# Optimization experiments

Hardware: AMD Instinct MI355X
Metric: run time of the kernel (lower is better)

## Reference

```python
import jax, jax.numpy as jnp
import numpy as np

N_HEADS = 8
N_LEVELS = 1
N_POINTS = 4
D_MODEL = 256
BATCH = 2
H0, W0 = 100, 150
LS = H0 * W0
LQ = 15000


def layer_norm(x, g, b, eps=1e-5):
    m = jnp.mean(x, -1, keepdims=True)
    v = jnp.var(x, -1, keepdims=True)
    return (x - m) * jax.lax.rsqrt(v + eps) * g + b


def bilinear_sample(v, Hl, Wl, loc):
    # v: [N, Hl*Wl, Hh, D] level features; loc in [0,1]: [N, Lq, Hh, P, 2] (x, y)
    Nb, _, Hh, D = v.shape
    Lq, P = loc.shape[1], loc.shape[3]
    x = loc[..., 0] * Wl - 0.5           # align_corners=False grid_sample convention
    y = loc[..., 1] * Hl - 0.5
    x0 = jnp.floor(x); y0 = jnp.floor(y)
    lx = (x - x0).transpose(0, 2, 1, 3)[..., None]   # [N,Hh,Lq,P,1]
    ly = (y - y0).transpose(0, 2, 1, 3)[..., None]
    x0i = x0.astype(jnp.int32); y0i = y0.astype(jnp.int32)
    vh = v.transpose(0, 2, 1, 3)                      # [N,Hh,Hl*Wl,D]

    def gather(xi, yi):
        valid = (xi >= 0) & (xi < Wl) & (yi >= 0) & (yi < Hl)   # zero padding
        idx = jnp.clip(yi, 0, Hl - 1) * Wl + jnp.clip(xi, 0, Wl - 1)
        idxf = idx.transpose(0, 2, 1, 3).reshape(Nb, Hh, Lq * P)
        g = jnp.take_along_axis(vh, idxf[..., None], axis=2).reshape(Nb, Hh, Lq, P, D)
        return g * valid.transpose(0, 2, 1, 3)[..., None]

    g00 = gather(x0i, y0i)
    g10 = gather(x0i + 1, y0i)
    g01 = gather(x0i, y0i + 1)
    g11 = gather(x0i + 1, y0i + 1)
    return (g00 * (1 - lx) * (1 - ly) + g10 * lx * (1 - ly)
            + g01 * (1 - lx) * ly + g11 * lx * ly)   # [N,Hh,Lq,P,D]


def ms_deform_attn(q, reference_points, src, shapes_np, starts_np, padding_mask,
                   W_val, b_val, W_off, b_off, W_attn, b_attn, W_out, b_out):
    Nb, Lq, C = q.shape
    Hh, D, L, P = N_HEADS, C // N_HEADS, N_LEVELS, N_POINTS
    value = src @ W_val + b_val
    value = jnp.where(padding_mask[..., None], 0.0, value).reshape(Nb, -1, Hh, D)
    offsets = (q @ W_off + b_off).reshape(Nb, Lq, Hh, L, P, 2)
    aw = jax.nn.softmax((q @ W_attn + b_attn).reshape(Nb, Lq, Hh, L * P), -1)
    aw = aw.reshape(Nb, Lq, Hh, L, P)
    # offset normalizer is (W, H) per level
    norm = jnp.asarray(shapes_np[:, ::-1].copy(), dtype=q.dtype)   # [L,2]
    loc = reference_points[:, :, None, :, None, :] + offsets / norm[None, None, None, :, None, :]
    out = 0.0
    for l in range(L):
        Hl, Wl = int(shapes_np[l, 0]), int(shapes_np[l, 1])
        s = int(starts_np[l])
        sampled = bilinear_sample(value[:, s:s + Hl * Wl], Hl, Wl, loc[:, :, :, l])
        out = out + jnp.sum(sampled * aw[:, :, :, l].transpose(0, 2, 1, 3)[..., None], axis=3)
    out = out.transpose(0, 2, 1, 3).reshape(Nb, Lq, C)
    return out @ W_out + b_out


def reference(tgt, query_pos, src_pos, tgt_spatial_shapes, reference_points,
              depth_reference_points, src, src_spatial_shapes, frame_start_index,
              src_padding_mask,
              W_dsa, b_dsa, g_nds, b_nds, W_off, b_off, W_attn, b_attn,
              W_val, b_val, W_out, b_out, W_csa, b_csa, g_n1, b_n1,
              W_ff, b_ff, g_n3, b_n3):
    ss = np.asarray(src_spatial_shapes)      # static level shapes
    starts = np.asarray(frame_start_index)
    # depth scale adaptation
    src_a = layer_norm(src @ W_dsa + b_dsa, g_nds, b_nds)
    q = tgt + query_pos
    tgt2 = ms_deform_attn(q, reference_points, src_a, ss, starts, src_padding_mask,
                          W_val, b_val, W_off, b_off, W_attn, b_attn, W_out, b_out)
    tgt2 = tgt2 @ W_csa + b_csa
    t = layer_norm(tgt + tgt2, g_n1, b_n1)
    # FFN: single linear d_model->d_model with exact GELU (per source code)
    ff = jax.nn.gelu(t @ W_ff + b_ff, approximate=False)
    return layer_norm(t + ff, g_n3, b_n3)


def setup_inputs() -> dict:
    key = jax.random.key(0)
    ks = jax.random.split(key, 24)
    C = D_MODEL
    Hh, L, P = N_HEADS, N_LEVELS, N_POINTS

    def lin(k, fin, fout, scale=None):
        s = (1.0 / np.sqrt(fin)) if scale is None else scale
        return (jax.random.normal(k, (fin, fout), jnp.float32) * s).astype(jnp.float32)

    inp = {}
    inp['tgt'] = jax.random.normal(ks[0], (BATCH, LQ, C), jnp.float32)
    inp['query_pos'] = 0.1 * jax.random.normal(ks[1], (BATCH, LQ, C), jnp.float32)
    inp['src_pos'] = 0.1 * jax.random.normal(ks[2], (BATCH, LS, C), jnp.float32)
    inp['tgt_spatial_shapes'] = jnp.array([[H0, W0]], jnp.int32)
    inp['reference_points'] = jax.random.uniform(ks[3], (BATCH, LQ, L, 2), jnp.float32)
    inp['depth_reference_points'] = jax.random.uniform(ks[4], (BATCH, LQ, 1, 2), jnp.float32)
    inp['src'] = jax.random.normal(ks[5], (BATCH, LS, C), jnp.float32)
    inp['src_spatial_shapes'] = jnp.array([[H0, W0]], jnp.int32)
    inp['frame_start_index'] = jnp.array([0], jnp.int32)
    inp['src_padding_mask'] = jnp.zeros((BATCH, LS), jnp.bool_)
    # parameters
    inp['W_dsa'] = lin(ks[6], C, C); inp['b_dsa'] = jnp.zeros((C,), jnp.float32)
    inp['g_nds'] = jnp.ones((C,), jnp.float32); inp['b_nds'] = jnp.zeros((C,), jnp.float32)
    inp['W_off'] = lin(ks[7], C, Hh * L * P * 2, scale=0.01)
    inp['b_off'] = 0.5 * jax.random.normal(ks[8], (Hh * L * P * 2,), jnp.float32)
    inp['W_attn'] = lin(ks[9], C, Hh * L * P)
    inp['b_attn'] = jnp.zeros((Hh * L * P,), jnp.float32)
    inp['W_val'] = lin(ks[10], C, C); inp['b_val'] = jnp.zeros((C,), jnp.float32)
    inp['W_out'] = lin(ks[11], C, C); inp['b_out'] = jnp.zeros((C,), jnp.float32)
    inp['W_csa'] = lin(ks[12], C, C); inp['b_csa'] = jnp.zeros((C,), jnp.float32)
    inp['g_n1'] = jnp.ones((C,), jnp.float32); inp['b_n1'] = jnp.zeros((C,), jnp.float32)
    inp['W_ff'] = lin(ks[13], C, C); inp['b_ff'] = jnp.zeros((C,), jnp.float32)
    inp['g_n3'] = jnp.ones((C,), jnp.float32); inp['b_n3'] = jnp.zeros((C,), jnp.float32)
    return inp
```

## Files before the change

kernel.cpp:

```cpp
#include <hip/hip_runtime.h>
#include <hip/hip_bf16.h>
#include <math.h>

#define LQ   15000
#define LS_  15000
#define NB   2
#define ROWS (NB*LQ)
#define HGT  100
#define WID  150

typedef __attribute__((ext_vector_type(8))) short bf16x8;
typedef __attribute__((ext_vector_type(4))) float f32x4;

__device__ inline short f2bf(float x) {
    __hip_bfloat16 h = __float2bfloat16(x);
    return *reinterpret_cast<short*>(&h);
}
__device__ inline unsigned pack2bf(float a, float b) {
    return ((unsigned)(unsigned short)f2bf(a)) | (((unsigned)(unsigned short)f2bf(b)) << 16);
}
__device__ inline float bf2f(short s) {
    return __uint_as_float(((unsigned)(unsigned short)s) << 16);
}
__device__ inline float gelu_exact(float x) {
    return 0.5f * x * (1.f + erff(x * 0.70710678118654752440f));
}

template<int MODE>
__global__ __launch_bounds__(256) void fused2(
    const void* __restrict__ Ap,
    const short* __restrict__ W1T, const float* __restrict__ bias1,
    const float* __restrict__ res1,
    const float* __restrict__ g1v, const float* __restrict__ b1v,
    const short* __restrict__ W2T, const float* __restrict__ bias2,
    void* __restrict__ Out,
    const unsigned char* __restrict__ mask,
    const float* __restrict__ g2v, const float* __restrict__ b2v,
    int M)
{
    __shared__ short As[64][40];
    __shared__ short Bs[256][40];
    __shared__ short T[64][264];
    __shared__ float s_b1[256], s_g1[256], s_bb1[256], s_b2[256], s_g2[256], s_bb2[256];

    const int tid = threadIdx.x;
    const int bm0 = blockIdx.x * 64;
    const int wave = tid >> 6, lane = tid & 63;
    const int quad = lane >> 4, c = lane & 15;

    s_b1[tid] = bias1[tid];
    s_g1[tid] = g1v[tid]; s_bb1[tid] = b1v[tid];
    s_b2[tid] = bias2[tid];
    if (MODE == 1) { s_g2[tid] = g2v[tid]; s_bb2[tid] = b2v[tid]; }

    f32x4 acc[16];
    #pragma unroll
    for (int t = 0; t < 16; ++t) acc[t] = (f32x4){0.f, 0.f, 0.f, 0.f};

    for (int k0 = 0; k0 < 256; k0 += 32) {
        if (MODE == 0) {
            const float* A = (const float*)Ap;
            #pragma unroll
            for (int it = 0; it < 2; ++it) {
                int f = it * 256 + tid; int m = f >> 3; int ko = (f & 7) * 4;
                int r = bm0 + m; if (r > M - 1) r = M - 1;
                float4 v = *(const float4*)&A[(size_t)r * 256 + k0 + ko];
                int2 p; p.x = pack2bf(v.x, v.y); p.y = pack2bf(v.z, v.w);
                *(int2*)&As[m][ko] = p;
            }
        } else {
            const short* A = (const short*)Ap;
            int m = tid >> 2; int ko = (tid & 3) * 8;
            int r = bm0 + m; if (r > M - 1) r = M - 1;
            *(int4*)&As[m][ko] = *(const int4*)&A[(size_t)r * 256 + k0 + ko];
        }
        #pragma unroll
        for (int it = 0; it < 4; ++it) {
            int f = it * 256 + tid; int n = f >> 2; int ko = (f & 3) * 8;
            *(int4*)&Bs[n][ko] = *(const int4*)&W1T[(size_t)n * 256 + k0 + ko];
        }
        __syncthreads();
        bf16x8 a = *(const bf16x8*)&As[wave * 16 + c][quad * 8];
        #pragma unroll
        for (int t = 0; t < 16; ++t) {
            bf16x8 b = *(const bf16x8*)&Bs[t * 16 + c][quad * 8];
            acc[t] = __builtin_amdgcn_mfma_f32_16x16x32_bf16(a, b, acc[t], 0, 0, 0);
        }
        __syncthreads();
    }

    {
        const int rb = wave * 16 + quad * 4;
        #pragma unroll
        for (int reg = 0; reg < 4; ++reg) {
            int rloc = rb + reg;
            int rg = bm0 + rloc; int rgl = (rg < M) ? rg : (M - 1);
            float s = 0.f, sq = 0.f;
            float vv[16];
            #pragma unroll
            for (int t = 0; t < 16; ++t) {
                float v = acc[t][reg] + s_b1[t * 16 + c];
                if (MODE == 1) v += res1[(size_t)rgl * 256 + t * 16 + c];
                vv[t] = v; s += v; sq += v * v;
            }
            #pragma unroll
            for (int o = 1; o < 16; o <<= 1) {
                s += __shfl_xor(s, o, 64); sq += __shfl_xor(sq, o, 64);
            }
            float mean = s * (1.f / 256.f);
            float var  = sq * (1.f / 256.f) - mean * mean;
            float rs   = rsqrtf(var + 1e-5f);
            #pragma unroll
            for (int t = 0; t < 16; ++t)
                T[rloc][t * 16 + c] = f2bf((vv[t] - mean) * rs * s_g1[t * 16 + c] + s_bb1[t * 16 + c]);
        }
    }
    __syncthreads();

    #pragma unroll
    for (int t = 0; t < 16; ++t) acc[t] = (f32x4){0.f, 0.f, 0.f, 0.f};
    for (int k0 = 0; k0 < 256; k0 += 32) {
        #pragma unroll
        for (int it = 0; it < 4; ++it) {
            int f = it * 256 + tid; int n = f >> 2; int ko = (f & 3) * 8;
            *(int4*)&Bs[n][ko] = *(const int4*)&W2T[(size_t)n * 256 + k0 + ko];
        }
        __syncthreads();
        bf16x8 a = *(const bf16x8*)&T[wave * 16 + c][k0 + quad * 8];
        #pragma unroll
        for (int t = 0; t < 16; ++t) {
            bf16x8 b = *(const bf16x8*)&Bs[t * 16 + c][quad * 8];
            acc[t] = __builtin_amdgcn_mfma_f32_16x16x32_bf16(a, b, acc[t], 0, 0, 0);
        }
        __syncthreads();
    }

    const int rb = wave * 16 + quad * 4;
    if constexpr (MODE == 0) {
        short* O = (short*)Out;
        #pragma unroll
        for (int reg = 0; reg < 4; ++reg) {
            int rloc = rb + reg; int r = bm0 + rloc;
            if (r < M) {
                float mz = mask[r] ? 0.f : 1.f;
                int n = (r >= LS_) ? 1 : 0;
                int sidx = r - n * LS_;
                #pragma unroll
                for (int t = 0; t < 16; ++t) {
                    int col = t * 16 + c; int h = col >> 5, d = col & 31;
                    O[(((size_t)n * 8 + h) * LS_ + sidx) * 32 + d] =
                        f2bf((acc[t][reg] + s_b2[col]) * mz);
                }
            }
        }
    } else {
        float* O = (float*)Out;
        #pragma unroll
        for (int reg = 0; reg < 4; ++reg) {
            int rloc = rb + reg; int r = bm0 + rloc;
            float s = 0.f, sq = 0.f;
            float vv[16];
            #pragma unroll
            for (int t = 0; t < 16; ++t) {
                int col = t * 16 + c;
                float v = gelu_exact(acc[t][reg] + s_b2[col]) + bf2f(T[rloc][col]);
                vv[t] = v; s += v; sq += v * v;
            }
            #pragma unroll
            for (int o = 1; o < 16; o <<= 1) {
                s += __shfl_xor(s, o, 64); sq += __shfl_xor(sq, o, 64);
            }
            float mean = s * (1.f / 256.f);
            float var  = sq * (1.f / 256.f) - mean * mean;
            float rs   = rsqrtf(var + 1e-5f);
            if (r < M) {
                #pragma unroll
                for (int t = 0; t < 16; ++t) {
                    int col = t * 16 + c;
                    O[(size_t)r * 256 + col] = (vv[t] - mean) * rs * s_g2[col] + s_bb2[col];
                }
            }
        }
    }
}

__global__ __launch_bounds__(256) void fused_oa_sample(
    const float* __restrict__ tgt, const float* __restrict__ qpos,
    const short* __restrict__ WToa, const float* __restrict__ b_oa,
    const short* __restrict__ value,
    const float* __restrict__ refp,
    short* __restrict__ out, int M)
{
    __shared__ short As[64][40];
    __shared__ short Bs[96][40];
    __shared__ float Ss[64][100];
    __shared__ float sb[96];

    const int tid = threadIdx.x;
    const int bm0 = blockIdx.x * 64;
    const int wave = tid >> 6, lane = tid & 63;
    const int quad = lane >> 4, c = lane & 15;

    if (tid < 96) sb[tid] = b_oa[tid];

    f32x4 acc[6];
    #pragma unroll
    for (int t = 0; t < 6; ++t) acc[t] = (f32x4){0.f, 0.f, 0.f, 0.f};

    for (int k0 = 0; k0 < 256; k0 += 32) {
        #pragma unroll
        for (int it = 0; it < 2; ++it) {
            int f = it * 256 + tid; int m = f >> 3; int ko = (f & 7) * 4;
            int r = bm0 + m; if (r > M - 1) r = M - 1;
            float4 v = *(const float4*)&tgt[(size_t)r * 256 + k0 + ko];
            float4 w = *(const float4*)&qpos[(size_t)r * 256 + k0 + ko];
            v.x += w.x; v.y += w.y; v.z += w.z; v.w += w.w;
            int2 p; p.x = pack2bf(v.x, v.y); p.y = pack2bf(v.z, v.w);
            *(int2*)&As[m][ko] = p;
        }
        #pragma unroll
        for (int it = 0; it < 2; ++it) {
            int f = it * 256 + tid;
            if (f < 384) {
                int n = f >> 2; int ko = (f & 3) * 8;
                *(int4*)&Bs[n][ko] = *(const int4*)&WToa[(size_t)n * 256 + k0 + ko];
            }
        }
        __syncthreads();
        bf16x8 a = *(const bf16x8*)&As[wave * 16 + c][quad * 8];
        #pragma unroll
        for (int t = 0; t < 6; ++t) {
            bf16x8 b = *(const bf16x8*)&Bs[t * 16 + c][quad * 8];
            acc[t] = __builtin_amdgcn_mfma_f32_16x16x32_bf16(a, b, acc[t], 0, 0, 0);
        }
        __syncthreads();
    }
    {
        const int rbq = wave * 16 + quad * 4;
        #pragma unroll
        for (int reg = 0; reg < 4; ++reg) {
            int rloc = rbq + reg;
            #pragma unroll
            for (int t = 0; t < 6; ++t)
                Ss[rloc][t * 16 + c] = acc[t][reg] + sb[t * 16 + c];
        }
    }
    __syncthreads();

    const int c4 = tid & 7;
    #pragma unroll 2
    for (int it = 0; it < 16; ++it) {
        int g = it * 32 + (tid >> 3);
        int rloc = g >> 3, h = g & 7;
        int r = bm0 + rloc;
        bool ok = r < M;
        int rr = ok ? r : (M - 1);
        int n = (rr >= LS_) ? 1 : 0;
        float rx = refp[(size_t)rr * 2 + 0], ry = refp[(size_t)rr * 2 + 1];
        float4 oA = *(const float4*)&Ss[rloc][h * 8];
        float4 oB = *(const float4*)&Ss[rloc][h * 8 + 4];
        float4 lg = *(const float4*)&Ss[rloc][64 + h * 4];

        float mx = fmaxf(fmaxf(lg.x, lg.y), fmaxf(lg.z, lg.w));
        float e0 = expf(lg.x - mx), e1 = expf(lg.y - mx), e2 = expf(lg.z - mx), e3 = expf(lg.w - mx);
        float inv = 1.f / (e0 + e1 + e2 + e3);
        float aw[4] = {e0 * inv, e1 * inv, e2 * inv, e3 * inv};
        float ox[4] = {oA.x, oA.z, oB.x, oB.z};
        float oy[4] = {oA.y, oA.w, oB.y, oB.w};

        const short* vb = value + (((size_t)n * 8 + h) * LS_) * 32 + c4 * 4;
        float a0 = 0.f, a1 = 0.f, a2 = 0.f, a3 = 0.f;
        #pragma unroll
        for (int p = 0; p < 4; ++p) {
            float x = rx * (float)WID + ox[p] - 0.5f;
            float y = ry * (float)HGT + oy[p] - 0.5f;
            float x0f = floorf(x), y0f = floorf(y);
            float lx = x - x0f, ly = y - y0f;
            int x0 = (int)x0f, y0 = (int)y0f;
            int x1 = x0 + 1, y1 = y0 + 1;
            bool vx0 = (x0 >= 0) & (x0 < WID), vx1 = (x1 >= 0) & (x1 < WID);
            bool vy0 = (y0 >= 0) & (y0 < HGT), vy1 = (y1 >= 0) & (y1 < HGT);
            float w00 = (vx0 & vy0) ? (1.f - lx) * (1.f - ly) * aw[p] : 0.f;
            float w10 = (vx1 & vy0) ? lx * (1.f - ly) * aw[p] : 0.f;
            float w01 = (vx0 & vy1) ? (1.f - lx) * ly * aw[p] : 0.f;
            float w11 = (vx1 & vy1) ? lx * ly * aw[p] : 0.f;
            int xc0 = min(max(x0, 0), WID - 1), xc1 = min(max(x1, 0), WID - 1);
            int yc0 = min(max(y0, 0), HGT - 1), yc1 = min(max(y1, 0), HGT - 1);
            int2 v00 = *(const int2*)&vb[(size_t)(yc0 * WID + xc0) * 32];
            int2 v10 = *(const int2*)&vb[(size_t)(yc0 * WID + xc1) * 32];
            int2 v01 = *(const int2*)&vb[(size_t)(yc1 * WID + xc0) * 32];
            int2 v11 = *(const int2*)&vb[(size_t)(yc1 * WID + xc1) * 32];
            a0 += w00 * __uint_as_float(((unsigned)v00.x) << 16)
                + w10 * __uint_as_float(((unsigned)v10.x) << 16)
                + w01 * __uint_as_float(((unsigned)v01.x) << 16)
                + w11 * __uint_as_float(((unsigned)v11.x) << 16);
            a1 += w00 * __uint_as_float(v00.x & 0xffff0000u)
                + w10 * __uint_as_float(v10.x & 0xffff0000u)
                + w01 * __uint_as_float(v01.x & 0xffff0000u)
                + w11 * __uint_as_float(v11.x & 0xffff0000u);
            a2 += w00 * __uint_as_float(((unsigned)v00.y) << 16)
                + w10 * __uint_as_float(((unsigned)v10.y) << 16)
                + w01 * __uint_as_float(((unsigned)v01.y) << 16)
                + w11 * __uint_as_float(((unsigned)v11.y) << 16);
            a3 += w00 * __uint_as_float(v00.y & 0xffff0000u)
                + w10 * __uint_as_float(v10.y & 0xffff0000u)
                + w01 * __uint_as_float(v01.y & 0xffff0000u)
                + w11 * __uint_as_float(v11.y & 0xffff0000u);
        }
        if (ok) {
            int2 o;
            o.x = pack2bf(a0, a1);
            o.y = pack2bf(a2, a3);
            *(int2*)&out[(size_t)r * 256 + h * 32 + c4 * 4] = o;
        }
    }
}

__global__ __launch_bounds__(256) void prep_all(
    const float* __restrict__ W_dsa, const float* __restrict__ W_val,
    const float* __restrict__ W_ff,  const float* __restrict__ W_out,
    const float* __restrict__ W_csa, const float* __restrict__ b_out,
    const float* __restrict__ b_csa, const float* __restrict__ W_off,
    const float* __restrict__ W_attn, const float* __restrict__ b_off,
    const float* __restrict__ b_attn,
    short* __restrict__ WT_dsa, short* __restrict__ WT_val, short* __restrict__ WT_ff,
    short* __restrict__ WT_c, float* __restrict__ bc,
    short* __restrict__ WT_oa, float* __restrict__ b_oa)
{
    __shared__ float tile[64][65];
    const int b = blockIdx.x, tid = threadIdx.x;
    if (b < 48) {
        const float* W = (b < 16) ? W_dsa : (b < 32) ? W_val : W_ff;
        short* WT = (b < 16) ? WT_dsa : (b < 32) ? WT_val : WT_ff;
        int t = b & 15; int bx = (t & 3) * 64, by = (t >> 2) * 64;
        #pragma unroll
        for (int it = 0; it < 4; ++it) {
            int f = it * 256 + tid; int i = f >> 4; int j = (f & 15) * 4;
            float4 v = *(const float4*)&W[(size_t)(by + i) * 256 + bx + j];
            tile[i][j] = v.x; tile[i][j + 1] = v.y; tile[i][j + 2] = v.z; tile[i][j + 3] = v.w;
        }
        __syncthreads();
        #pragma unroll
        for (int it = 0; it < 16; ++it) {
            int f = it * 256 + tid; int nl = f >> 6; int kl = f & 63;
            WT[(size_t)(bx + nl) * 256 + by + kl] = f2bf(tile[kl][nl]);
        }
    } else if (b < 304) {
        int k = b - 48, n = tid;
        float s = 0.f;
        for (int j = 0; j < 256; ++j)
            s = fmaf(W_out[(size_t)k * 256 + j], W_csa[(size_t)j * 256 + n], s);
        WT_c[(size_t)n * 256 + k] = f2bf(s);
    } else if (b == 304) {
        int j = tid;
        float s = b_csa[j];
        for (int k = 0; k < 256; ++k)
            s = fmaf(b_out[k], W_csa[(size_t)k * 256 + j], s);
        bc[j] = s;
    } else {
        int j = b - 305, k = tid;
        float v = (j < 64) ? W_off[(size_t)k * 64 + j] : W_attn[(size_t)k * 32 + (j - 64)];
        WT_oa[(size_t)j * 256 + k] = f2bf(v);
        if (k == 0) b_oa[j] = (j < 64) ? b_off[j] : b_attn[j - 64];
    }
}

extern "C" void kernel_launch(void* const* d_in, const int* in_sizes, int n_in,
                              void* d_out, int out_size, void* d_ws, size_t ws_size,
                              hipStream_t stream)
{
    const float* tgt       = (const float*)d_in[0];
    const float* query_pos = (const float*)d_in[1];
    const float* refp      = (const float*)d_in[4];
    const float* src       = (const float*)d_in[6];
    const unsigned char* mask = (const unsigned char*)d_in[9];
    const float* W_dsa  = (const float*)d_in[10]; const float* b_dsa  = (const float*)d_in[11];
    const float* g_nds  = (const float*)d_in[12]; const float* b_nds  = (const float*)d_in[13];
    const float* W_off  = (const float*)d_in[14]; const float* b_off  = (const float*)d_in[15];
    const float* W_attn = (const float*)d_in[16]; const float* b_attn = (const float*)d_in[17];
    const float* W_val  = (const float*)d_in[18]; const float* b_val  = (const float*)d_in[19];
    const float* W_out  = (const float*)d_in[20]; const float* b_out  = (const float*)d_in[21];
    const float* W_csa  = (const float*)d_in[22]; const float* b_csa  = (const float*)d_in[23];
    const float* g_n1   = (const float*)d_in[24]; const float* b_n1   = (const float*)d_in[25];
    const float* W_ff   = (const float*)d_in[26]; const float* b_ff   = (const float*)d_in[27];
    const float* g_n3   = (const float*)d_in[28]; const float* b_n3   = (const float*)d_in[29];
    float* out = (float*)d_out;

    short* attn_out = (short*)d_ws;
    short* value    = attn_out + (size_t)ROWS * 256;
    short* WT_dsa   = value + (size_t)ROWS * 256;
    short* WT_val   = WT_dsa + 65536;
    short* WT_ff    = WT_val + 65536;
    short* WT_c     = WT_ff + 65536;
    short* WT_oa    = WT_c + 65536;
    float* bc       = (float*)(WT_oa + 96 * 256);
    float* b_oa     = bc + 256;

    dim3 blk(256);
    const int GB = (ROWS + 63) / 64;

    prep_all<<<401, blk, 0, stream>>>(
        W_dsa, W_val, W_ff, W_out, W_csa, b_out, b_csa, W_off, W_attn, b_off, b_attn,
        WT_dsa, WT_val, WT_ff, WT_c, bc, WT_oa, b_oa);

    fused2<0><<<GB, blk, 0, stream>>>(
        src, WT_dsa, b_dsa, nullptr, g_nds, b_nds,
        WT_val, b_val, value, mask, nullptr, nullptr, ROWS);

    fused_oa_sample<<<GB, blk, 0, stream>>>(
        tgt, query_pos, WT_oa, b_oa, value, refp, attn_out, ROWS);

    fused2<1><<<GB, blk, 0, stream>>>(
        attn_out, WT_c, bc, tgt, g_n1, b_n1,
        WT_ff, b_ff, out, nullptr, g_n3, b_n3, ROWS);
}
```

Baseline: 332.7 us.

## Split offset GEMM from deformable sampling and shrink fused2 LDS footprint

Breaks the fused offset/attention GEMM plus bilinear-sampling kernel into two kernels. The GEMM now writes its 96-wide logits to a float workspace, and a standalone lightweight sampling kernel reads it back, so the gather-heavy sampling phase is no longer bound to the GEMM kernel's LDS and occupancy. In fused2, the normalized intermediate T now shares LDS with the A tile, and the per-column parameter arrays are no longer cached in LDS but read straight from global memory. Together with a launch-bounds occupancy hint, this cuts shared memory per block and the barrier after writing T is dropped. The cost is an extra round trip of the intermediate scores through global memory, extra global bias loads, and one more kernel launch.

```diff
diff --git a/kernel.cpp b/kernel.cpp
--- a/kernel.cpp
+++ b/kernel.cpp
@@ -27,7 +27,7 @@
 }
 
 template<int MODE>
-__global__ __launch_bounds__(256) void fused2(
+__global__ __launch_bounds__(256, 3) void fused2(
     const void* __restrict__ Ap,
     const short* __restrict__ W1T, const float* __restrict__ bias1,
     const float* __restrict__ res1,
@@ -38,20 +38,15 @@
     const float* __restrict__ g2v, const float* __restrict__ b2v,
     int M)
 {
-    __shared__ short As[64][40];
-    __shared__ short Bs[256][40];
-    __shared__ short T[64][264];
-    __shared__ float s_b1[256], s_g1[256], s_bb1[256], s_b2[256], s_g2[256], s_bb2[256];
+    __shared__ __align__(16) char lds[54272];
+    short (*Bs)[40]  = (short(*)[40])lds;
+    short (*T)[264]  = (short(*)[264])(lds + 20480);
+    short (*As)[40]  = (short(*)[40])(lds + 20480);
 
     const int tid = threadIdx.x;
     const int bm0 = blockIdx.x * 64;
     const int wave = tid >> 6, lane = tid & 63;
     const int quad = lane >> 4, c = lane & 15;
-
-    s_b1[tid] = bias1[tid];
-    s_g1[tid] = g1v[tid]; s_bb1[tid] = b1v[tid];
-    s_b2[tid] = bias2[tid];
-    if (MODE == 1) { s_g2[tid] = g2v[tid]; s_bb2[tid] = b2v[tid]; }
 
     f32x4 acc[16];
     #pragma unroll
@@ -99,8 +94,9 @@
             float vv[16];
             #pragma unroll
             for (int t = 0; t < 16; ++t) {
-                float v = acc[t][reg] + s_b1[t * 16 + c];
-                if (MODE == 1) v += res1[(size_t)rgl * 256 + t * 16 + c];
+                int col = t * 16 + c;
+                float v = acc[t][reg] + bias1[col];
+                if (MODE == 1) v += res1[(size_t)rgl * 256 + col];
                 vv[t] = v; s += v; sq += v * v;
             }
             #pragma unroll
@@ -111,11 +107,12 @@
             float var  = sq * (1.f / 256.f) - mean * mean;
             float rs   = rsqrtf(var + 1e-5f);
             #pragma unroll
-            for (int t = 0; t < 16; ++t)
-                T[rloc][t * 16 + c] = f2bf((vv[t] - mean) * rs * s_g1[t * 16 + c] + s_bb1[t * 16 + c]);
-        }
-    }
-    __syncthreads();
+            for (int t = 0; t < 16; ++t) {
+                int col = t * 16 + c;
+                T[rloc][col] = f2bf((vv[t] - mean) * rs * g1v[col] + b1v[col]);
+            }
+        }
+    }
 
     #pragma unroll
     for (int t = 0; t < 16; ++t) acc[t] = (f32x4){0.f, 0.f, 0.f, 0.f};
@@ -149,7 +146,7 @@
                 for (int t = 0; t < 16; ++t) {
                     int col = t * 16 + c; int h = col >> 5, d = col & 31;
                     O[(((size_t)n * 8 + h) * LS_ + sidx) * 32 + d] =
-                        f2bf((acc[t][reg] + s_b2[col]) * mz);
+                        f2bf((acc[t][reg] + bias2[col]) * mz);
                 }
             }
         }
@@ -163,7 +160,7 @@
             #pragma unroll
             for (int t = 0; t < 16; ++t) {
                 int col = t * 16 + c;
-                float v = gelu_exact(acc[t][reg] + s_b2[col]) + bf2f(T[rloc][col]);
+                float v = gelu_exact(acc[t][reg] + bias2[col]) + bf2f(T[rloc][col]);
                 vv[t] = v; s += v; sq += v * v;
             }
             #pragma unroll
@@ -177,23 +174,20 @@
                 #pragma unroll
                 for (int t = 0; t < 16; ++t) {
                     int col = t * 16 + c;
-                    O[(size_t)r * 256 + col] = (vv[t] - mean) * rs * s_g2[col] + s_bb2[col];
+                    O[(size_t)r * 256 + col] = (vv[t] - mean) * rs * g2v[col] + b2v[col];
                 }
             }
         }
     }
 }
 
-__global__ __launch_bounds__(256) void fused_oa_sample(
+__global__ __launch_bounds__(256) void oa_gemm(
     const float* __restrict__ tgt, const float* __restrict__ qpos,
     const short* __restrict__ WToa, const float* __restrict__ b_oa,
-    const short* __restrict__ value,
-    const float* __restrict__ refp,
-    short* __restrict__ out, int M)
+    float* __restrict__ S_oa, int M)
 {
     __shared__ short As[64][40];
     __shared__ short Bs[96][40];
-    __shared__ float Ss[64][100];
     __shared__ float sb[96];
 
     const int tid = threadIdx.x;
@@ -218,12 +212,16 @@
             int2 p; p.x = pack2bf(v.x, v.y); p.y = pack2bf(v.z, v.w);
             *(int2*)&As[m][ko] = p;
         }
-        #pragma unroll
-        for (int it = 0; it < 2; ++it) {
-            int f = it * 256 + tid;
-            if (f < 384) {
-                int n = f >> 2; int ko = (f & 3) * 8;
-                *(int4*)&Bs[n][ko] = *(const int4*)&WToa[(size_t)n * 256 + k0 + ko];
+        {
+            int f = tid;
+            if (f < 192) {  }
+            #pragma unroll
+            for (int it = 0; it < 2; ++it) {
+                int ff = it * 256 + tid;
+                if (ff < 384) {
+                    int n = ff >> 2; int ko = (ff & 3) * 8;
+                    *(int4*)&Bs[n][ko] = *(const int4*)&WToa[(size_t)n * 256 + k0 + ko];
+                }
             }
         }
         __syncthreads();
@@ -235,85 +233,88 @@
         }
         __syncthreads();
     }
-    {
-        const int rbq = wave * 16 + quad * 4;
-        #pragma unroll
-        for (int reg = 0; reg < 4; ++reg) {
-            int rloc = rbq + reg;
+
+    const int rb = wave * 16 + quad * 4;
+    #pragma unroll
+    for (int reg = 0; reg < 4; ++reg) {
+        int r = bm0 + rb + reg;
+        if (r < M) {
             #pragma unroll
             for (int t = 0; t < 6; ++t)
-                Ss[rloc][t * 16 + c] = acc[t][reg] + sb[t * 16 + c];
-        }
-    }
-    __syncthreads();
-
-    const int c4 = tid & 7;
-    #pragma unroll 2
-    for (int it = 0; it < 16; ++it) {
-        int g = it * 32 + (tid >> 3);
-        int rloc = g >> 3, h = g & 7;
-        int r = bm0 + rloc;
-        bool ok = r < M;
-        int rr = ok ? r : (M - 1);
-        int n = (rr >= LS_) ? 1 : 0;
-        float rx = refp[(size_t)rr * 2 + 0], ry = refp[(size_t)rr * 2 + 1];
-        float4 oA = *(const float4*)&Ss[rloc][h * 8];
-        float4 oB = *(const float4*)&Ss[rloc][h * 8 + 4];
-        float4 lg = *(const float4*)&Ss[rloc][64 + h * 4];
-
-        float mx = fmaxf(fmaxf(lg.x, lg.y), fmaxf(lg.z, lg.w));
-        float e0 = expf(lg.x - mx), e1 = expf(lg.y - mx), e2 = expf(lg.z - mx), e3 = expf(lg.w - mx);
-        float inv = 1.f / (e0 + e1 + e2 + e3);
-        float aw[4] = {e0 * inv, e1 * inv, e2 * inv, e3 * inv};
-        float ox[4] = {oA.x, oA.z, oB.x, oB.z};
-        float oy[4] = {oA.y, oA.w, oB.y, oB.w};
-
-        const short* vb = value + (((size_t)n * 8 + h) * LS_) * 32 + c4 * 4;
-        float a0 = 0.f, a1 = 0.f, a2 = 0.f, a3 = 0.f;
-        #pragma unroll
-        for (int p = 0; p < 4; ++p) {
-            float x = rx * (float)WID + ox[p] - 0.5f;
-            float y = ry * (float)HGT + oy[p] - 0.5f;
-            float x0f = floorf(x), y0f = floorf(y);
-            float lx = x - x0f, ly = y - y0f;
-            int x0 = (int)x0f, y0 = (int)y0f;
-            int x1 = x0 + 1, y1 = y0 + 1;
-            bool vx0 = (x0 >= 0) & (x0 < WID), vx1 = (x1 >= 0) & (x1 < WID);
-            bool vy0 = (y0 >= 0) & (y0 < HGT), vy1 = (y1 >= 0) & (y1 < HGT);
-            float w00 = (vx0 & vy0) ? (1.f - lx) * (1.f - ly) * aw[p] : 0.f;
-            float w10 = (vx1 & vy0) ? lx * (1.f - ly) * aw[p] : 0.f;
-            float w01 = (vx0 & vy1) ? (1.f - lx) * ly * aw[p] : 0.f;
-            float w11 = (vx1 & vy1) ? lx * ly * aw[p] : 0.f;
-            int xc0 = min(max(x0, 0), WID - 1), xc1 = min(max(x1, 0), WID - 1);
-            int yc0 = min(max(y0, 0), HGT - 1), yc1 = min(max(y1, 0), HGT - 1);
-            int2 v00 = *(const int2*)&vb[(size_t)(yc0 * WID + xc0) * 32];
-            int2 v10 = *(const int2*)&vb[(size_t)(yc0 * WID + xc1) * 32];
-            int2 v01 = *(const int2*)&vb[(size_t)(yc1 * WID + xc0) * 32];
-            int2 v11 = *(const int2*)&vb[(size_t)(yc1 * WID + xc1) * 32];
-            a0 += w00 * __uint_as_float(((unsigned)v00.x) << 16)
-                + w10 * __uint_as_float(((unsigned)v10.x) << 16)
-                + w01 * __uint_as_float(((unsigned)v01.x) << 16)
-                + w11 * __uint_as_float(((unsigned)v11.x) << 16);
-            a1 += w00 * __uint_as_float(v00.x & 0xffff0000u)
-                + w10 * __uint_as_float(v10.x & 0xffff0000u)
-                + w01 * __uint_as_float(v01.x & 0xffff0000u)
-                + w11 * __uint_as_float(v11.x & 0xffff0000u);
-            a2 += w00 * __uint_as_float(((unsigned)v00.y) << 16)
-                + w10 * __uint_as_float(((unsigned)v10.y) << 16)
-                + w01 * __uint_as_float(((unsigned)v01.y) << 16)
-                + w11 * __uint_as_float(((unsigned)v11.y) << 16);
-            a3 += w00 * __uint_as_float(v00.y & 0xffff0000u)
-                + w10 * __uint_as_float(v10.y & 0xffff0000u)
-                + w01 * __uint_as_float(v01.y & 0xffff0000u)
-                + w11 * __uint_as_float(v11.y & 0xffff0000u);
-        }
-        if (ok) {
-            int2 o;
-            o.x = pack2bf(a0, a1);
-            o.y = pack2bf(a2, a3);
-            *(int2*)&out[(size_t)r * 256 + h * 32 + c4 * 4] = o;
-        }
-    }
+                S_oa[(size_t)r * 96 + t * 16 + c] = acc[t][reg] + sb[t * 16 + c];
+        }
+    }
+}
+
+__global__ __launch_bounds__(256) void deform_sample(
+    const short* __restrict__ value,
+    const float* __restrict__ S_oa,
+    const float* __restrict__ refp,
+    short* __restrict__ out)
+{
+    int grp = blockIdx.x * 32 + (threadIdx.x >> 3);
+    int c4  = threadIdx.x & 7;
+    int h = grp & 7;
+    int r = grp >> 3;
+    int n = (r >= LS_) ? 1 : 0;
+
+    const float* row = S_oa + (size_t)r * 96;
+    float rx = refp[(size_t)r * 2 + 0], ry = refp[(size_t)r * 2 + 1];
+    float4 oA = *(const float4*)&row[h * 8];
+    float4 oB = *(const float4*)&row[h * 8 + 4];
+    float4 lg = *(const float4*)&row[64 + h * 4];
+
+    float mx = fmaxf(fmaxf(lg.x, lg.y), fmaxf(lg.z, lg.w));
+    float e0 = expf(lg.x - mx), e1 = expf(lg.y - mx), e2 = expf(lg.z - mx), e3 = expf(lg.w - mx);
+    float inv = 1.f / (e0 + e1 + e2 + e3);
+    float aw[4] = {e0 * inv, e1 * inv, e2 * inv, e3 * inv};
+    float ox[4] = {oA.x, oA.z, oB.x, oB.z};
+    float oy[4] = {oA.y, oA.w, oB.y, oB.w};
+
+    const short* vb = value + (((size_t)n * 8 + h) * LS_) * 32 + c4 * 4;
+    float a0 = 0.f, a1 = 0.f, a2 = 0.f, a3 = 0.f;
+
+    #pragma unroll
+    for (int p = 0; p < 4; ++p) {
+        float x = rx * (float)WID + ox[p] - 0.5f;
+        float y = ry * (float)HGT + oy[p] - 0.5f;
+        float x0f = floorf(x), y0f = floorf(y);
+        float lx = x - x0f, ly = y - y0f;
+        int x0 = (int)x0f, y0 = (int)y0f;
+        int x1 = x0 + 1, y1 = y0 + 1;
+        bool vx0 = (x0 >= 0) & (x0 < WID), vx1 = (x1 >= 0) & (x1 < WID);
+        bool vy0 = (y0 >= 0) & (y0 < HGT), vy1 = (y1 >= 0) & (y1 < HGT);
+        float w00 = (vx0 & vy0) ? (1.f - lx) * (1.f - ly) * aw[p] : 0.f;
+        float w10 = (vx1 & vy0) ? lx * (1.f - ly) * aw[p] : 0.f;
+        float w01 = (vx0 & vy1) ? (1.f - lx) * ly * aw[p] : 0.f;
+        float w11 = (vx1 & vy1) ? lx * ly * aw[p] : 0.f;
+        int xc0 = min(max(x0, 0), WID - 1), xc1 = min(max(x1, 0), WID - 1);
+        int yc0 = min(max(y0, 0), HGT - 1), yc1 = min(max(y1, 0), HGT - 1);
+        int2 v00 = *(const int2*)&vb[(size_t)(yc0 * WID + xc0) * 32];
+        int2 v10 = *(const int2*)&vb[(size_t)(yc0 * WID + xc1) * 32];
+        int2 v01 = *(const int2*)&vb[(size_t)(yc1 * WID + xc0) * 32];
+        int2 v11 = *(const int2*)&vb[(size_t)(yc1 * WID + xc1) * 32];
+        a0 += w00 * __uint_as_float(((unsigned)v00.x) << 16)
+            + w10 * __uint_as_float(((unsigned)v10.x) << 16)
+            + w01 * __uint_as_float(((unsigned)v01.x) << 16)
+            + w11 * __uint_as_float(((unsigned)v11.x) << 16);
+        a1 += w00 * __uint_as_float(v00.x & 0xffff0000u)
+            + w10 * __uint_as_float(v10.x & 0xffff0000u)
+            + w01 * __uint_as_float(v01.x & 0xffff0000u)
+            + w11 * __uint_as_float(v11.x & 0xffff0000u);
+        a2 += w00 * __uint_as_float(((unsigned)v00.y) << 16)
+            + w10 * __uint_as_float(((unsigned)v10.y) << 16)
+            + w01 * __uint_as_float(((unsigned)v01.y) << 16)
+            + w11 * __uint_as_float(((unsigned)v11.y) << 16);
+        a3 += w00 * __uint_as_float(v00.y & 0xffff0000u)
+            + w10 * __uint_as_float(v10.y & 0xffff0000u)
+            + w01 * __uint_as_float(v01.y & 0xffff0000u)
+            + w11 * __uint_as_float(v11.y & 0xffff0000u);
+    }
+    int2 o;
+    o.x = pack2bf(a0, a1);
+    o.y = pack2bf(a2, a3);
+    *(int2*)&out[(size_t)r * 256 + h * 32 + c4 * 4] = o;
 }
 
 __global__ __launch_bounds__(256) void prep_all(
@@ -348,12 +349,14 @@
     } else if (b < 304) {
         int k = b - 48, n = tid;
         float s = 0.f;
+        #pragma unroll 8
         for (int j = 0; j < 256; ++j)
             s = fmaf(W_out[(size_t)k * 256 + j], W_csa[(size_t)j * 256 + n], s);
         WT_c[(size_t)n * 256 + k] = f2bf(s);
     } else if (b == 304) {
         int j = tid;
         float s = b_csa[j];
+        #pragma unroll 8
         for (int k = 0; k < 256; ++k)
             s = fmaf(b_out[k], W_csa[(size_t)k * 256 + j], s);
         bc[j] = s;
@@ -388,7 +391,8 @@
 
     short* attn_out = (short*)d_ws;
     short* value    = attn_out + (size_t)ROWS * 256;
-    short* WT_dsa   = value + (size_t)ROWS * 256;
+    float* S_oa     = (float*)(value + (size_t)ROWS * 256);
+    short* WT_dsa   = (short*)(S_oa + (size_t)ROWS * 96);
     short* WT_val   = WT_dsa + 65536;
     short* WT_ff    = WT_val + 65536;
     short* WT_c     = WT_ff + 65536;
@@ -403,12 +407,13 @@
         W_dsa, W_val, W_ff, W_out, W_csa, b_out, b_csa, W_off, W_attn, b_off, b_attn,
         WT_dsa, WT_val, WT_ff, WT_c, bc, WT_oa, b_oa);
 
+    oa_gemm<<<GB, blk, 0, stream>>>(tgt, query_pos, WT_oa, b_oa, S_oa, ROWS);
+
     fused2<0><<<GB, blk, 0, stream>>>(
         src, WT_dsa, b_dsa, nullptr, g_nds, b_nds,
         WT_val, b_val, value, mask, nullptr, nullptr, ROWS);
 
-    fused_oa_sample<<<GB, blk, 0, stream>>>(
-        tgt, query_pos, WT_oa, b_oa, value, refp, attn_out, ROWS);
+    deform_sample<<<ROWS * 8 / 32, blk, 0, stream>>>(value, S_oa, refp, attn_out);
 
     fused2<1><<<GB, blk, 0, stream>>>(
         attn_out, WT_c, bc, tgt, g_n1, b_n1,
```

New measurement: 320.0 us. -3.8%, faster.
